# Performance work log

Measured on AMD Instinct MI355X. Metric: run time of the kernel, lower is better.

## Reference

```python
import jax, jax.numpy as jnp
import numpy as np

HIDDEN = 1024
B, S = 4, 2048

def setup_inputs() -> dict:
    key = jax.random.key(0)
    ks = jax.random.split(key, 8)
    scale = 1.0 / np.sqrt(HIDDEN)
    return {
        "x": jax.random.normal(ks[0], (B, S, HIDDEN), dtype=jnp.float32),
        "mask": jax.random.randint(ks[1], (B, S, S), 0, 2, dtype=jnp.int32),
        "Wq": jax.random.normal(ks[2], (HIDDEN, HIDDEN), dtype=jnp.float32) * scale,
        "bq": jax.random.normal(ks[3], (HIDDEN,), dtype=jnp.float32) * 0.01,
        "Wk": jax.random.normal(ks[4], (HIDDEN, HIDDEN), dtype=jnp.float32) * scale,
        "bk": jax.random.normal(ks[5], (HIDDEN,), dtype=jnp.float32) * 0.01,
        "Wv": jax.random.normal(ks[6], (HIDDEN, HIDDEN), dtype=jnp.float32) * scale,
        "bv": jax.random.normal(ks[7], (HIDDEN,), dtype=jnp.float32) * 0.01,
    }

def reference(x, mask, Wq, bq, Wk, bk, Wv, bv):
    # torch Linear: y = x @ W.T + b
    Q = jnp.einsum("bsh,oh->bso", x, Wq) + bq
    K = jnp.einsum("bsh,oh->bso", x, Wk) + bk
    V = jnp.einsum("bsh,oh->bso", x, Wv) + bv
    inv_sqrt_h = 1.0 / jnp.sqrt(jnp.asarray(Q.shape[-1], Q.dtype))
    score = jnp.einsum("bqh,bkh->bqk", Q, K) * inv_sqrt_h  # [B, S, S]
    score = jnp.where(mask == 0, jnp.asarray(-jnp.inf, score.dtype), score)
    attn = jax.nn.softmax(score, axis=-1)
    return jnp.einsum("bqk,bkh->bqh", attn, V)
```

## Files before the change

### kernel.cpp

```cpp
#include <hip/hip_runtime.h>

using u16 = unsigned short;
using u32 = unsigned int;

typedef __attribute__((ext_vector_type(4))) float f32x4;
typedef __attribute__((ext_vector_type(8))) short s16x8;

__device__ __forceinline__ u16 f2b(float f) {
  u32 u = __builtin_bit_cast(u32, f);
  u += 0x7FFFu + ((u >> 16) & 1u);
  return (u16)(u >> 16);
}
__device__ __forceinline__ float b2f(u16 h) {
  return __builtin_bit_cast(float, (u32)h << 16);
}
__device__ __forceinline__ void gl_lds16(const void* g, void* l) {
  __builtin_amdgcn_global_load_lds(
      (const __attribute__((address_space(1))) void*)g,
      (__attribute__((address_space(3))) void*)l, 16, 0, 0);
}

__global__ __launch_bounds__(256) void convert4_k(
    const float* __restrict__ x, const float* __restrict__ Wq,
    const float* __restrict__ Wk, const float* __restrict__ Wv,
    u16* __restrict__ dst) {
  long g = (long)(blockIdx.x * 256 + threadIdx.x) * 8;
  const float* s;
  if (g < 8388608L)       s = x  + g;
  else if (g < 9437184L)  s = Wq + (g - 8388608L);
  else if (g < 10485760L) s = Wk + (g - 9437184L);
  else                    s = Wv + (g - 10485760L);
  f32x4 lo = *(const f32x4*)s;
  f32x4 hi = *(const f32x4*)(s + 4);
  s16x8 o;
  #pragma unroll
  for (int e = 0; e < 4; ++e) { o[e] = (short)f2b(lo[e]); o[4 + e] = (short)f2b(hi[e]); }
  *(s16x8*)(dst + g) = o;
}

template<int EPI>
__global__ __launch_bounds__(256) void gemm_bt(
    const u16* __restrict__ A, const u16* __restrict__ B0,
    const u16* __restrict__ W2, const u16* __restrict__ W3,
    int lda, int ldb, int K, long za, long zb, long ze,
    const float* __restrict__ bq, const float* __restrict__ bk, const float* __restrict__ bv,
    u16* __restrict__ qw, u16* __restrict__ kw, u16* __restrict__ vt,
    const int* __restrict__ mask, u16* __restrict__ sc, float* __restrict__ outO)
{
  __shared__ __align__(16) u16 lds[128 * 64 * 2];
  const int tid = threadIdx.x;
  const int wave = tid >> 6, lane = tid & 63;
  const int wr = wave >> 1, wc = wave & 1;
  const int m0 = blockIdx.y * 128, n0 = blockIdx.x * 128;
  const long z = blockIdx.z;
  A += z * za;

  const u16* Bsrc = B0;
  int nbase = n0;
  if constexpr (EPI == 0) {
    Bsrc = (n0 < 1024) ? B0 : (n0 < 2048) ? W2 : W3;
    nbase = n0 & 1023;
  }
  Bsrc += z * zb;

  u16* As = lds;
  u16* Bs = lds + 128 * 64;

  f32x4 acc[4][4];
  const f32x4 fz = {0.f, 0.f, 0.f, 0.f};
  #pragma unroll
  for (int i = 0; i < 4; ++i)
    #pragma unroll
    for (int j = 0; j < 4; ++j) acc[i][j] = fz;

  const int frow = lane & 15;
  const int q    = lane >> 4;

  for (int k0 = 0; k0 < K; k0 += 64) {
    __syncthreads();
    #pragma unroll
    for (int call = 0; call < 4; ++call) {
      int c = call * 256 + tid;
      int row = c >> 3;
      int kc  = (c & 7) ^ (row & 7);
      const u16* ga = A    + (size_t)(m0    + row) * lda + (k0 + kc * 8);
      const u16* gb = Bsrc + (size_t)(nbase + row) * ldb + (k0 + kc * 8);
      gl_lds16(ga, As + (size_t)c * 8);
      gl_lds16(gb, Bs + (size_t)c * 8);
    }
    __syncthreads();

    #pragma unroll
    for (int t = 0; t < 2; ++t) {
      s16x8 af[4], bf[4];
      #pragma unroll
      for (int i = 0; i < 4; ++i) {
        int lr = wr * 64 + i * 16 + frow;
        af[i] = *(const s16x8*)(As + lr * 64 + (((t * 4 + q) ^ (lr & 7)) << 3));
      }
      #pragma unroll
      for (int j = 0; j < 4; ++j) {
        int lc = wc * 64 + j * 16 + frow;
        bf[j] = *(const s16x8*)(Bs + lc * 64 + (((t * 4 + q) ^ (lc & 7)) << 3));
      }
      #pragma unroll
      for (int i = 0; i < 4; ++i)
        #pragma unroll
        for (int j = 0; j < 4; ++j)
          acc[i][j] = __builtin_amdgcn_mfma_f32_16x16x32_bf16(af[i], bf[j], acc[i][j], 0, 0, 0);
    }
  }

  const int r0 = (lane >> 4) * 4;
  const int ccol = lane & 15;
  #pragma unroll
  for (int i = 0; i < 4; ++i) {
    #pragma unroll
    for (int j = 0; j < 4; ++j) {
      #pragma unroll
      for (int r = 0; r < 4; ++r) {
        int R = m0 + wr * 64 + i * 16 + r0 + r;
        int C = n0 + wc * 64 + j * 16 + ccol;
        float v = acc[i][j][r];
        if constexpr (EPI == 0) {
          int sec = C >> 10, nl = C & 1023;
          v += (sec == 0) ? bq[nl] : (sec == 1) ? bk[nl] : bv[nl];
          u16 o = f2b(v);
          int b = R >> 11, s = R & 2047;
          if (sec == 0)      qw[(size_t)R * 1024 + nl] = o;
          else if (sec == 1) kw[(size_t)R * 1024 + nl] = o;
          else               vt[(size_t)b * 2097152u + (size_t)nl * 2048 + s] = o;
        } else if constexpr (EPI == 1) {
          v *= 0.03125f;
          size_t idx = (size_t)(z * ze) + (size_t)R * 2048 + C;
          if (mask[idx] == 0) v = -__builtin_inff();
          sc[idx] = f2b(v);
        } else {
          outO[(size_t)(z * ze) + (size_t)R * 1024 + C] = v;
        }
      }
    }
  }
}

__global__ __launch_bounds__(256) void softmax_k(u16* __restrict__ Sc) {
  __shared__ float red[8];
  u16* p = Sc + (size_t)blockIdx.x * 2048;
  const int tid = threadIdx.x;
  const int lane = tid & 63, wv = tid >> 6;
  s16x8 u = *(const s16x8*)(p + tid * 8);
  float v[8];
  #pragma unroll
  for (int e = 0; e < 8; ++e) v[e] = b2f((u16)u[e]);
  float mx = v[0];
  #pragma unroll
  for (int e = 1; e < 8; ++e) mx = fmaxf(mx, v[e]);
  #pragma unroll
  for (int off = 32; off > 0; off >>= 1) mx = fmaxf(mx, __shfl_xor(mx, off));
  if (lane == 0) red[wv] = mx;
  __syncthreads();
  mx = fmaxf(fmaxf(red[0], red[1]), fmaxf(red[2], red[3]));
  float s = 0.f;
  #pragma unroll
  for (int e = 0; e < 8; ++e) { v[e] = __expf(v[e] - mx); s += v[e]; }
  #pragma unroll
  for (int off = 32; off > 0; off >>= 1) s += __shfl_xor(s, off);
  if (lane == 0) red[4 + wv] = s;
  __syncthreads();
  s = (red[4] + red[5]) + (red[6] + red[7]);
  float inv = 1.f / s;
  s16x8 o;
  #pragma unroll
  for (int e = 0; e < 8; ++e) o[e] = (short)f2b(v[e] * inv);
  *(s16x8*)(p + tid * 8) = o;
}

extern "C" void kernel_launch(void* const* d_in, const int* in_sizes, int n_in,
                              void* d_out, int out_size, void* d_ws, size_t ws_size,
                              hipStream_t stream) {
  const float* x  = (const float*)d_in[0];
  const int* mask = (const int*)d_in[1];
  const float* Wq = (const float*)d_in[2];
  const float* bq = (const float*)d_in[3];
  const float* Wk = (const float*)d_in[4];
  const float* bk = (const float*)d_in[5];
  const float* Wv = (const float*)d_in[6];
  const float* bv = (const float*)d_in[7];
  float* out = (float*)d_out;
  char* ws = (char*)d_ws;

  u16* xc  = (u16*)ws;
  u16* Wqc = (u16*)(ws + (16u << 20));
  u16* Wkc = (u16*)(ws + (18u << 20));
  u16* Wvc = (u16*)(ws + (20u << 20));
  u16* Qw  = (u16*)(ws + (22u << 20));
  u16* Kw  = (u16*)(ws + (38u << 20));
  u16* Vt  = (u16*)(ws + (54u << 20));
  u16* Sc  = (u16*)(ws + (70u << 20));

  convert4_k<<<5632, 256, 0, stream>>>(x, Wq, Wk, Wv, xc);

  gemm_bt<0><<<dim3(24, 64, 1), 256, 0, stream>>>(
      xc, Wqc, Wkc, Wvc, 1024, 1024, 1024, 0, 0, 0,
      bq, bk, bv, Qw, Kw, Vt, nullptr, nullptr, nullptr);
  gemm_bt<1><<<dim3(16, 16, 4), 256, 0, stream>>>(
      Qw, Kw, nullptr, nullptr, 1024, 1024, 1024, 2097152, 2097152, 4194304,
      nullptr, nullptr, nullptr, nullptr, nullptr, nullptr, mask, Sc, nullptr);
  softmax_k<<<8192, 256, 0, stream>>>(Sc);
  gemm_bt<2><<<dim3(8, 16, 4), 256, 0, stream>>>(
      Sc, Vt, nullptr, nullptr, 2048, 2048, 2048, 4194304, 2097152, 2097152,
      nullptr, nullptr, nullptr, nullptr, nullptr, nullptr, nullptr, nullptr, out);
}
```

Measured before the change: 345.6 us.

## Rewrite GEMM with 4-stage async LDS pipeline, 512-thread blocks, 256-wide tiles

Replaces the single-buffered 128x128 GEMM with a 512-thread kernel that uses 256-column tiles, a per-instantiation row count (128 or 256), and K-step 32. Four LDS buffers are filled ahead with global_load_lds, and explicit vmcnt waits with raw barriers let loads for tile T+3 overlap compute on tile T. It also precomputes global and LDS addresses and raises wave priority around the MFMA block. The cost targeted is load latency exposed by the old sync-load-sync-compute loop. In exchange, grids are smaller, occupancy depends on fitting two blocks per CU, and correctness relies on the hand-written vmcnt counts.

```diff
diff --git a/kernel.cpp b/kernel.cpp
--- a/kernel.cpp
+++ b/kernel.cpp
@@ -18,6 +18,18 @@
   __builtin_amdgcn_global_load_lds(
       (const __attribute__((address_space(1))) void*)g,
       (__attribute__((address_space(3))) void*)l, 16, 0, 0);
+}
+template<int N> __device__ __forceinline__ void waitvm() {
+  static_assert(N == 8 || N == 6 || N == 4 || N == 3 || N == 0, "literal");
+  if constexpr (N == 8)      asm volatile("s_waitcnt vmcnt(8)" ::: "memory");
+  else if constexpr (N == 6) asm volatile("s_waitcnt vmcnt(6)" ::: "memory");
+  else if constexpr (N == 4) asm volatile("s_waitcnt vmcnt(4)" ::: "memory");
+  else if constexpr (N == 3) asm volatile("s_waitcnt vmcnt(3)" ::: "memory");
+  else                       asm volatile("s_waitcnt vmcnt(0)" ::: "memory");
+}
+__device__ __forceinline__ void barrier_np() {
+  __builtin_amdgcn_s_barrier();
+  asm volatile("" ::: "memory");
 }
 
 __global__ __launch_bounds__(256) void convert4_k(
@@ -38,8 +50,8 @@
   *(s16x8*)(dst + g) = o;
 }
 
-template<int EPI>
-__global__ __launch_bounds__(256) void gemm_bt(
+template<int EPI, int MREP>
+__global__ __launch_bounds__(512, 2) void gemm_nt(
     const u16* __restrict__ A, const u16* __restrict__ B0,
     const u16* __restrict__ W2, const u16* __restrict__ W3,
     int lda, int ldb, int K, long za, long zb, long ze,
@@ -47,11 +59,17 @@
     u16* __restrict__ qw, u16* __restrict__ kw, u16* __restrict__ vt,
     const int* __restrict__ mask, u16* __restrict__ sc, float* __restrict__ outO)
 {
-  __shared__ __align__(16) u16 lds[128 * 64 * 2];
-  const int tid = threadIdx.x;
+  constexpr int BM    = 32 * MREP;
+  constexpr int ACH   = BM * 4;
+  constexpr int CH    = ACH + 1024;
+  constexpr int CALLS = CH / 512;
+  constexpr int BUF   = CH * 8;
+  __shared__ __align__(16) u16 lds[4 * BUF];
+
+  const int tid  = threadIdx.x;
   const int wave = tid >> 6, lane = tid & 63;
-  const int wr = wave >> 1, wc = wave & 1;
-  const int m0 = blockIdx.y * 128, n0 = blockIdx.x * 128;
+  const int wr = wave >> 2, wc = wave & 3;
+  const int m0 = blockIdx.y * BM, n0 = blockIdx.x * 256;
   const long z = blockIdx.z;
   A += z * za;
 
@@ -63,63 +81,84 @@
   }
   Bsrc += z * zb;
 
-  u16* As = lds;
-  u16* Bs = lds + 128 * 64;
-
-  f32x4 acc[4][4];
-  const f32x4 fz = {0.f, 0.f, 0.f, 0.f};
-  #pragma unroll
-  for (int i = 0; i < 4; ++i)
-    #pragma unroll
-    for (int j = 0; j < 4; ++j) acc[i][j] = fz;
+  const u16* gsrc[CALLS];
+  u32 loff[CALLS];
+  #pragma unroll
+  for (int call = 0; call < CALLS; ++call) {
+    int qq  = call * 512 + tid;
+    int isB = qq >= ACH;
+    int r   = (isB ? qq - ACH : qq) >> 2;
+    int kc  = (qq & 3) ^ (r & 3);
+    gsrc[call] = isB ? (Bsrc + (size_t)(nbase + r) * ldb + kc * 8)
+                     : (A    + (size_t)(m0    + r) * lda + kc * 8);
+    loff[call] = (u32)qq * 8;
+  }
 
   const int frow = lane & 15;
   const int q    = lane >> 4;
-
-  for (int k0 = 0; k0 < K; k0 += 64) {
-    __syncthreads();
-    #pragma unroll
-    for (int call = 0; call < 4; ++call) {
-      int c = call * 256 + tid;
-      int row = c >> 3;
-      int kc  = (c & 7) ^ (row & 7);
-      const u16* ga = A    + (size_t)(m0    + row) * lda + (k0 + kc * 8);
-      const u16* gb = Bsrc + (size_t)(nbase + row) * ldb + (k0 + kc * 8);
-      gl_lds16(ga, As + (size_t)c * 8);
-      gl_lds16(gb, Bs + (size_t)c * 8);
+  u32 aoff[MREP], boff[4];
+  #pragma unroll
+  for (int i = 0; i < MREP; ++i) {
+    int lr = wr * (16 * MREP) + i * 16 + frow;
+    aoff[i] = (u32)lr * 32 + (u32)((q ^ (lr & 3)) << 3);
+  }
+  #pragma unroll
+  for (int j = 0; j < 4; ++j) {
+    int lc = wc * 64 + j * 16 + frow;
+    boff[j] = (u32)ACH * 8 + (u32)lc * 32 + (u32)((q ^ (lc & 3)) << 3);
+  }
+
+  f32x4 acc[MREP][4];
+  const f32x4 fz = {0.f, 0.f, 0.f, 0.f};
+  #pragma unroll
+  for (int i = 0; i < MREP; ++i)
+    #pragma unroll
+    for (int j = 0; j < 4; ++j) acc[i][j] = fz;
+
+  const int NT = K >> 5;
+
+  auto stage = [&](int t) {
+    u16* buf = lds + (size_t)(t & 3) * BUF;
+    #pragma unroll
+    for (int call = 0; call < CALLS; ++call)
+      gl_lds16(gsrc[call] + (size_t)t * 32, buf + loff[call]);
+  };
+  auto comp = [&](int t) {
+    const u16* buf = lds + (size_t)(t & 3) * BUF;
+    s16x8 bf[4];
+    #pragma unroll
+    for (int j = 0; j < 4; ++j) bf[j] = *(const s16x8*)(buf + boff[j]);
+    __builtin_amdgcn_s_setprio(1);
+    #pragma unroll
+    for (int i = 0; i < MREP; ++i) {
+      s16x8 af = *(const s16x8*)(buf + aoff[i]);
+      #pragma unroll
+      for (int j = 0; j < 4; ++j)
+        acc[i][j] = __builtin_amdgcn_mfma_f32_16x16x32_bf16(af, bf[j], acc[i][j], 0, 0, 0);
     }
-    __syncthreads();
-
-    #pragma unroll
-    for (int t = 0; t < 2; ++t) {
-      s16x8 af[4], bf[4];
-      #pragma unroll
-      for (int i = 0; i < 4; ++i) {
-        int lr = wr * 64 + i * 16 + frow;
-        af[i] = *(const s16x8*)(As + lr * 64 + (((t * 4 + q) ^ (lr & 7)) << 3));
-      }
-      #pragma unroll
-      for (int j = 0; j < 4; ++j) {
-        int lc = wc * 64 + j * 16 + frow;
-        bf[j] = *(const s16x8*)(Bs + lc * 64 + (((t * 4 + q) ^ (lc & 7)) << 3));
-      }
-      #pragma unroll
-      for (int i = 0; i < 4; ++i)
-        #pragma unroll
-        for (int j = 0; j < 4; ++j)
-          acc[i][j] = __builtin_amdgcn_mfma_f32_16x16x32_bf16(af[i], bf[j], acc[i][j], 0, 0, 0);
-    }
-  }
+    __builtin_amdgcn_s_setprio(0);
+  };
+
+  stage(0); stage(1); stage(2);
+  for (int T = 0; T < NT - 3; ++T) {
+    waitvm<2 * CALLS>();
+    barrier_np();
+    stage(T + 3);
+    comp(T);
+  }
+  waitvm<2 * CALLS>(); barrier_np(); comp(NT - 3);
+  waitvm<CALLS>();     barrier_np(); comp(NT - 2);
+  waitvm<0>();         barrier_np(); comp(NT - 1);
 
   const int r0 = (lane >> 4) * 4;
   const int ccol = lane & 15;
   #pragma unroll
-  for (int i = 0; i < 4; ++i) {
+  for (int i = 0; i < MREP; ++i) {
     #pragma unroll
     for (int j = 0; j < 4; ++j) {
       #pragma unroll
       for (int r = 0; r < 4; ++r) {
-        int R = m0 + wr * 64 + i * 16 + r0 + r;
+        int R = m0 + wr * (16 * MREP) + i * 16 + r0 + r;
         int C = n0 + wc * 64 + j * 16 + ccol;
         float v = acc[i][j][r];
         if constexpr (EPI == 0) {
@@ -200,14 +239,14 @@
 
   convert4_k<<<5632, 256, 0, stream>>>(x, Wq, Wk, Wv, xc);
 
-  gemm_bt<0><<<dim3(24, 64, 1), 256, 0, stream>>>(
+  gemm_nt<0, 4><<<dim3(12, 64, 1), 512, 0, stream>>>(
       xc, Wqc, Wkc, Wvc, 1024, 1024, 1024, 0, 0, 0,
       bq, bk, bv, Qw, Kw, Vt, nullptr, nullptr, nullptr);
-  gemm_bt<1><<<dim3(16, 16, 4), 256, 0, stream>>>(
+  gemm_nt<1, 8><<<dim3(8, 8, 4), 512, 0, stream>>>(
       Qw, Kw, nullptr, nullptr, 1024, 1024, 1024, 2097152, 2097152, 4194304,
       nullptr, nullptr, nullptr, nullptr, nullptr, nullptr, mask, Sc, nullptr);
   softmax_k<<<8192, 256, 0, stream>>>(Sc);
-  gemm_bt<2><<<dim3(8, 16, 4), 256, 0, stream>>>(
+  gemm_nt<2, 4><<<dim3(4, 16, 4), 512, 0, stream>>>(
       Sc, Vt, nullptr, nullptr, 2048, 2048, 2048, 4194304, 2097152, 2097152,
       nullptr, nullptr, nullptr, nullptr, nullptr, nullptr, nullptr, nullptr, out);
 }
```

After: 338.6 us. 2.0% less time.

## Triple-buffer GEMM K-loop with async LDS loads and wider score-GEMM tiles

Applied to the files above, without the earlier changes.

Replaces the GEMM's single-buffered 64-wide K loop, which synchronised twice per step, with a three-slot ring of 32-wide K tiles. Global-to-LDS loads for tile T+2 are issued before computing tile T, and vmcnt waits plus a bare barrier replace full syncthreads. It precomputes per-thread load and fragment offsets, raises MFMA issue priority, and uses a 128x256 tile with 512 threads for the QK^T GEMM. The aim is to hide global load latency behind MFMA work, at the cost of more LDS and more registers, which could reduce occupancy.

```diff
diff --git a/kernel.cpp b/kernel.cpp
--- a/kernel.cpp
+++ b/kernel.cpp
@@ -18,6 +18,16 @@
   __builtin_amdgcn_global_load_lds(
       (const __attribute__((address_space(1))) void*)g,
       (__attribute__((address_space(3))) void*)l, 16, 0, 0);
+}
+template<int N> __device__ __forceinline__ void waitvm() {
+  static_assert(N == 4 || N == 3 || N == 0, "literal");
+  if constexpr (N == 4)      asm volatile("s_waitcnt vmcnt(4)" ::: "memory");
+  else if constexpr (N == 3) asm volatile("s_waitcnt vmcnt(3)" ::: "memory");
+  else                       asm volatile("s_waitcnt vmcnt(0)" ::: "memory");
+}
+__device__ __forceinline__ void barrier_np() {
+  __builtin_amdgcn_s_barrier();
+  asm volatile("" ::: "memory");
 }
 
 __global__ __launch_bounds__(256) void convert4_k(
@@ -38,8 +48,8 @@
   *(s16x8*)(dst + g) = o;
 }
 
-template<int EPI>
-__global__ __launch_bounds__(256) void gemm_bt(
+template<int EPI, int NWC>
+__global__ __launch_bounds__(128 * NWC, 2) void gemm_nt(
     const u16* __restrict__ A, const u16* __restrict__ B0,
     const u16* __restrict__ W2, const u16* __restrict__ W3,
     int lda, int ldb, int K, long za, long zb, long ze,
@@ -47,11 +57,19 @@
     u16* __restrict__ qw, u16* __restrict__ kw, u16* __restrict__ vt,
     const int* __restrict__ mask, u16* __restrict__ sc, float* __restrict__ outO)
 {
-  __shared__ __align__(16) u16 lds[128 * 64 * 2];
-  const int tid = threadIdx.x;
+  constexpr int THREADS = 128 * NWC;
+  constexpr int LOGW    = (NWC == 2) ? 1 : 2;
+  constexpr int BN      = 64 * NWC;
+  constexpr int ACH     = 512;
+  constexpr int CH      = ACH + BN * 4;
+  constexpr int CALLS   = CH / THREADS;
+  constexpr int SLOT    = CH * 8;
+  __shared__ __align__(16) u16 lds[3 * SLOT];
+
+  const int tid  = threadIdx.x;
   const int wave = tid >> 6, lane = tid & 63;
-  const int wr = wave >> 1, wc = wave & 1;
-  const int m0 = blockIdx.y * 128, n0 = blockIdx.x * 128;
+  const int wr = wave >> LOGW, wc = wave & (NWC - 1);
+  const int m0 = blockIdx.y * 128, n0 = blockIdx.x * BN;
   const long z = blockIdx.z;
   A += z * za;
 
@@ -63,8 +81,32 @@
   }
   Bsrc += z * zb;
 
-  u16* As = lds;
-  u16* Bs = lds + 128 * 64;
+  const u16* gsrc[CALLS];
+  u32 loff[CALLS];
+  #pragma unroll
+  for (int c = 0; c < CALLS; ++c) {
+    int qq  = c * THREADS + tid;
+    int isB = qq >= ACH;
+    int r   = (isB ? qq - ACH : qq) >> 2;
+    int kc  = (qq & 3) ^ ((r >> 1) & 3);
+    gsrc[c] = (isB ? (Bsrc + (size_t)(nbase + r) * ldb)
+                   : (A    + (size_t)(m0    + r) * lda)) + kc * 8;
+    loff[c] = (u32)qq * 8;
+  }
+
+  const int frow = lane & 15;
+  const int q    = lane >> 4;
+  u32 aoff[4], boff[4];
+  #pragma unroll
+  for (int i = 0; i < 4; ++i) {
+    int lr = wr * 64 + i * 16 + frow;
+    aoff[i] = (u32)lr * 32 + (u32)((q ^ ((lr >> 1) & 3)) << 3);
+  }
+  #pragma unroll
+  for (int j = 0; j < 4; ++j) {
+    int lc = wc * 64 + j * 16 + frow;
+    boff[j] = (u32)ACH * 8 + (u32)lc * 32 + (u32)((q ^ ((lc >> 1) & 3)) << 3);
+  }
 
   f32x4 acc[4][4];
   const f32x4 fz = {0.f, 0.f, 0.f, 0.f};
@@ -73,43 +115,43 @@
     #pragma unroll
     for (int j = 0; j < 4; ++j) acc[i][j] = fz;
 
-  const int frow = lane & 15;
-  const int q    = lane >> 4;
-
-  for (int k0 = 0; k0 < K; k0 += 64) {
-    __syncthreads();
-    #pragma unroll
-    for (int call = 0; call < 4; ++call) {
-      int c = call * 256 + tid;
-      int row = c >> 3;
-      int kc  = (c & 7) ^ (row & 7);
-      const u16* ga = A    + (size_t)(m0    + row) * lda + (k0 + kc * 8);
-      const u16* gb = Bsrc + (size_t)(nbase + row) * ldb + (k0 + kc * 8);
-      gl_lds16(ga, As + (size_t)c * 8);
-      gl_lds16(gb, Bs + (size_t)c * 8);
-    }
-    __syncthreads();
-
-    #pragma unroll
-    for (int t = 0; t < 2; ++t) {
-      s16x8 af[4], bf[4];
+  const int NT = K >> 5;
+
+  auto tile_compute = [&](const u16* buf) {
+    s16x8 bf[4], af[4];
+    #pragma unroll
+    for (int j = 0; j < 4; ++j) bf[j] = *(const s16x8*)(buf + boff[j]);
+    #pragma unroll
+    for (int i = 0; i < 4; ++i) af[i] = *(const s16x8*)(buf + aoff[i]);
+    __builtin_amdgcn_s_setprio(1);
+    #pragma unroll
+    for (int i = 0; i < 4; ++i)
       #pragma unroll
-      for (int i = 0; i < 4; ++i) {
-        int lr = wr * 64 + i * 16 + frow;
-        af[i] = *(const s16x8*)(As + lr * 64 + (((t * 4 + q) ^ (lr & 7)) << 3));
-      }
-      #pragma unroll
-      for (int j = 0; j < 4; ++j) {
-        int lc = wc * 64 + j * 16 + frow;
-        bf[j] = *(const s16x8*)(Bs + lc * 64 + (((t * 4 + q) ^ (lc & 7)) << 3));
-      }
-      #pragma unroll
-      for (int i = 0; i < 4; ++i)
-        #pragma unroll
-        for (int j = 0; j < 4; ++j)
-          acc[i][j] = __builtin_amdgcn_mfma_f32_16x16x32_bf16(af[i], bf[j], acc[i][j], 0, 0, 0);
-    }
-  }
+      for (int j = 0; j < 4; ++j)
+        acc[i][j] = __builtin_amdgcn_mfma_f32_16x16x32_bf16(af[i], bf[j], acc[i][j], 0, 0, 0);
+    __builtin_amdgcn_s_setprio(0);
+  };
+
+  #pragma unroll
+  for (int c = 0; c < CALLS; ++c) gl_lds16(gsrc[c],      lds        + loff[c]);
+  #pragma unroll
+  for (int c = 0; c < CALLS; ++c) gl_lds16(gsrc[c] + 32, lds + SLOT + loff[c]);
+
+  int rd = 0, st = 2;
+  for (int T = 0; T < NT - 2; ++T) {
+    waitvm<CALLS>();
+    barrier_np();
+    u16* sb = lds + (size_t)st * SLOT;
+    const size_t koff = (size_t)(T + 2) * 32;
+    #pragma unroll
+    for (int c = 0; c < CALLS; ++c) gl_lds16(gsrc[c] + koff, sb + loff[c]);
+    tile_compute(lds + (size_t)rd * SLOT);
+    rd = (rd == 2) ? 0 : rd + 1;
+    st = (st == 2) ? 0 : st + 1;
+  }
+  waitvm<CALLS>(); barrier_np(); tile_compute(lds + (size_t)rd * SLOT);
+  rd = (rd == 2) ? 0 : rd + 1;
+  waitvm<0>();     barrier_np(); tile_compute(lds + (size_t)rd * SLOT);
 
   const int r0 = (lane >> 4) * 4;
   const int ccol = lane & 15;
@@ -200,14 +242,14 @@
 
   convert4_k<<<5632, 256, 0, stream>>>(x, Wq, Wk, Wv, xc);
 
-  gemm_bt<0><<<dim3(24, 64, 1), 256, 0, stream>>>(
+  gemm_nt<0, 2><<<dim3(24, 64, 1), 256, 0, stream>>>(
       xc, Wqc, Wkc, Wvc, 1024, 1024, 1024, 0, 0, 0,
       bq, bk, bv, Qw, Kw, Vt, nullptr, nullptr, nullptr);
-  gemm_bt<1><<<dim3(16, 16, 4), 256, 0, stream>>>(
+  gemm_nt<1, 4><<<dim3(8, 16, 4), 512, 0, stream>>>(
       Qw, Kw, nullptr, nullptr, 1024, 1024, 1024, 2097152, 2097152, 4194304,
       nullptr, nullptr, nullptr, nullptr, nullptr, nullptr, mask, Sc, nullptr);
   softmax_k<<<8192, 256, 0, stream>>>(Sc);
-  gemm_bt<2><<<dim3(8, 16, 4), 256, 0, stream>>>(
+  gemm_nt<2, 2><<<dim3(8, 16, 4), 256, 0, stream>>>(
       Sc, Vt, nullptr, nullptr, 2048, 2048, 2048, 4194304, 2097152, 2097152,
       nullptr, nullptr, nullptr, nullptr, nullptr, nullptr, nullptr, nullptr, out);
 }
```

Result: faster. 331.7 us (-4.0%).

## Pipeline GEMM with triple-buffered B in LDS, direct-register A, XCD remap

Applied to the files above, without the earlier changes.

Rewrites the GEMM main loop to use a K-step of 32 with a three-slot LDS ring for the B tile, issued two steps ahead. The A fragments now load straight from global memory into registers, double-buffered, instead of going through LDS. Explicit vmcnt waits and a single barrier per step replace the two __syncthreads per step. Workgroups are remapped so neighbouring tiles land on the same XCD, and MFMA issue priority is raised. The aim is to overlap global loads with MFMA work and to improve L2 locality, at the cost of A loads that are not staged or shared across waves, more registers, and manual waitcnt logic that must stay correct.

```diff
diff --git a/kernel.cpp b/kernel.cpp
--- a/kernel.cpp
+++ b/kernel.cpp
@@ -18,6 +18,24 @@
   __builtin_amdgcn_global_load_lds(
       (const __attribute__((address_space(1))) void*)g,
       (__attribute__((address_space(3))) void*)l, 16, 0, 0);
+}
+template<int N> __device__ __forceinline__ void waitvm() {
+  static_assert(N == 2 || N == 0, "literal");
+  if constexpr (N == 2) asm volatile("s_waitcnt vmcnt(2)" ::: "memory");
+  else                  asm volatile("s_waitcnt vmcnt(0)" ::: "memory");
+}
+__device__ __forceinline__ void barrier_np() {
+  __builtin_amdgcn_s_barrier();
+  asm volatile("" ::: "memory");
+}
+
+__device__ __forceinline__ void xcd_remap(int& bx, int& by, int& bz) {
+  const int gx = (int)gridDim.x, gy = (int)gridDim.y;
+  const int nwg = gx * gy * (int)gridDim.z;
+  int flat = ((int)blockIdx.z * gy + (int)blockIdx.y) * gx + (int)blockIdx.x;
+  flat = (flat & 7) * (nwg >> 3) + (flat >> 3);
+  bx = flat % gx; flat /= gx;
+  by = flat % gy; bz = flat / gy;
 }
 
 __global__ __launch_bounds__(256) void convert4_k(
@@ -39,7 +57,7 @@
 }
 
 template<int EPI>
-__global__ __launch_bounds__(256) void gemm_bt(
+__global__ __launch_bounds__(256, 3) void gemm_nt(
     const u16* __restrict__ A, const u16* __restrict__ B0,
     const u16* __restrict__ W2, const u16* __restrict__ W3,
     int lda, int ldb, int K, long za, long zb, long ze,
@@ -47,12 +65,18 @@
     u16* __restrict__ qw, u16* __restrict__ kw, u16* __restrict__ vt,
     const int* __restrict__ mask, u16* __restrict__ sc, float* __restrict__ outO)
 {
-  __shared__ __align__(16) u16 lds[128 * 64 * 2];
-  const int tid = threadIdx.x;
+  constexpr int BCH  = 512;
+  constexpr int SLOT = BCH * 8;
+  __shared__ __align__(16) u16 lds[3 * SLOT];
+
+  int bx, by, bz;
+  xcd_remap(bx, by, bz);
+
+  const int tid  = threadIdx.x;
   const int wave = tid >> 6, lane = tid & 63;
   const int wr = wave >> 1, wc = wave & 1;
-  const int m0 = blockIdx.y * 128, n0 = blockIdx.x * 128;
-  const long z = blockIdx.z;
+  const int m0 = by * 128, n0 = bx * 128;
+  const long z = bz;
   A += z * za;
 
   const u16* Bsrc = B0;
@@ -63,8 +87,31 @@
   }
   Bsrc += z * zb;
 
-  u16* As = lds;
-  u16* Bs = lds + 128 * 64;
+  const u16* gsrcB[2];
+  u32 loffB[2];
+  #pragma unroll
+  for (int c = 0; c < 2; ++c) {
+    int qq = c * 256 + tid;
+    int r  = qq >> 2;
+    int kc = (qq & 3) ^ ((r >> 1) & 3);
+    gsrcB[c] = Bsrc + (size_t)(nbase + r) * ldb + kc * 8;
+    loffB[c] = (u32)qq * 8;
+  }
+
+  const int frow = lane & 15;
+  const int q    = lane >> 4;
+
+  const u16* pAf[4];
+  #pragma unroll
+  for (int i = 0; i < 4; ++i)
+    pAf[i] = A + (size_t)(m0 + wr * 64 + i * 16 + frow) * lda + q * 8;
+
+  u32 boff[4];
+  #pragma unroll
+  for (int j = 0; j < 4; ++j) {
+    int lc = wc * 64 + j * 16 + frow;
+    boff[j] = (u32)lc * 32 + (u32)((q ^ ((lc >> 1) & 3)) << 3);
+  }
 
   f32x4 acc[4][4];
   const f32x4 fz = {0.f, 0.f, 0.f, 0.f};
@@ -73,42 +120,45 @@
     #pragma unroll
     for (int j = 0; j < 4; ++j) acc[i][j] = fz;
 
-  const int frow = lane & 15;
-  const int q    = lane >> 4;
-
-  for (int k0 = 0; k0 < K; k0 += 64) {
-    __syncthreads();
-    #pragma unroll
-    for (int call = 0; call < 4; ++call) {
-      int c = call * 256 + tid;
-      int row = c >> 3;
-      int kc  = (c & 7) ^ (row & 7);
-      const u16* ga = A    + (size_t)(m0    + row) * lda + (k0 + kc * 8);
-      const u16* gb = Bsrc + (size_t)(nbase + row) * ldb + (k0 + kc * 8);
-      gl_lds16(ga, As + (size_t)c * 8);
-      gl_lds16(gb, Bs + (size_t)c * 8);
-    }
-    __syncthreads();
-
-    #pragma unroll
-    for (int t = 0; t < 2; ++t) {
-      s16x8 af[4], bf[4];
-      #pragma unroll
-      for (int i = 0; i < 4; ++i) {
-        int lr = wr * 64 + i * 16 + frow;
-        af[i] = *(const s16x8*)(As + lr * 64 + (((t * 4 + q) ^ (lr & 7)) << 3));
-      }
-      #pragma unroll
-      for (int j = 0; j < 4; ++j) {
-        int lc = wc * 64 + j * 16 + frow;
-        bf[j] = *(const s16x8*)(Bs + lc * 64 + (((t * 4 + q) ^ (lc & 7)) << 3));
-      }
+  const int NT = K >> 5;
+
+  auto stageB = [&](int t) {
+    u16* sb = lds + (size_t)(t % 3) * SLOT;
+    #pragma unroll
+    for (int c = 0; c < 2; ++c) gl_lds16(gsrcB[c] + (size_t)t * 32, sb + loffB[c]);
+  };
+  auto loadA = [&](int t, s16x8 (&d)[4]) {
+    #pragma unroll
+    for (int i = 0; i < 4; ++i) d[i] = *(const s16x8*)(pAf[i] + (size_t)t * 32);
+  };
+
+  s16x8 fa[4], ga[4];
+  loadA(0, fa);
+  stageB(0); stageB(1);
+
+  auto body = [&](int T, s16x8 (&ca)[4], s16x8 (&na)[4]) {
+    if (T < NT - 1) waitvm<2>(); else waitvm<0>();
+    barrier_np();
+    if (T + 1 < NT) loadA(T + 1, na);
+    __builtin_amdgcn_sched_barrier(0);
+    if (T + 2 < NT) stageB(T + 2);
+    __builtin_amdgcn_sched_barrier(0);
+    const u16* buf = lds + (size_t)(T % 3) * SLOT;
+    s16x8 bf[4];
+    #pragma unroll
+    for (int j = 0; j < 4; ++j) bf[j] = *(const s16x8*)(buf + boff[j]);
+    __builtin_amdgcn_s_setprio(1);
+    #pragma unroll
+    for (int j = 0; j < 4; ++j)
       #pragma unroll
       for (int i = 0; i < 4; ++i)
-        #pragma unroll
-        for (int j = 0; j < 4; ++j)
-          acc[i][j] = __builtin_amdgcn_mfma_f32_16x16x32_bf16(af[i], bf[j], acc[i][j], 0, 0, 0);
-    }
+        acc[i][j] = __builtin_amdgcn_mfma_f32_16x16x32_bf16(ca[i], bf[j], acc[i][j], 0, 0, 0);
+    __builtin_amdgcn_s_setprio(0);
+  };
+
+  for (int T = 0; T < NT; T += 2) {
+    body(T,     fa, ga);
+    body(T + 1, ga, fa);
   }
 
   const int r0 = (lane >> 4) * 4;
@@ -200,14 +250,14 @@
 
   convert4_k<<<5632, 256, 0, stream>>>(x, Wq, Wk, Wv, xc);
 
-  gemm_bt<0><<<dim3(24, 64, 1), 256, 0, stream>>>(
+  gemm_nt<0><<<dim3(24, 64, 1), 256, 0, stream>>>(
       xc, Wqc, Wkc, Wvc, 1024, 1024, 1024, 0, 0, 0,
       bq, bk, bv, Qw, Kw, Vt, nullptr, nullptr, nullptr);
-  gemm_bt<1><<<dim3(16, 16, 4), 256, 0, stream>>>(
+  gemm_nt<1><<<dim3(16, 16, 4), 256, 0, stream>>>(
       Qw, Kw, nullptr, nullptr, 1024, 1024, 1024, 2097152, 2097152, 4194304,
       nullptr, nullptr, nullptr, nullptr, nullptr, nullptr, mask, Sc, nullptr);
   softmax_k<<<8192, 256, 0, stream>>>(Sc);
-  gemm_bt<2><<<dim3(8, 16, 4), 256, 0, stream>>>(
+  gemm_nt<2><<<dim3(8, 16, 4), 256, 0, stream>>>(
       Sc, Vt, nullptr, nullptr, 2048, 2048, 2048, 4194304, 2097152, 2097152,
       nullptr, nullptr, nullptr, nullptr, nullptr, nullptr, nullptr, nullptr, out);
 }
```

New measurement: 437.9 us. 26.7% more time.
